# Kernel optimization log

Measured on AMD Instinct MI355X. Metric: run time of the kernel, lower is better.

Reference implementation:

```python
import jax, jax.numpy as jnp
import numpy as np

E, L, M, F, S, P = 4, 10, 512, 128, 1000, 10  # envs, labels, max_sample, features, sample_size, batch_len


def setup_inputs() -> dict:
    key = jax.random.key(0)
    k1, k2, k3 = jax.random.split(key, 3)
    data_len = jax.random.randint(k1, (E, L), M // 2, M + 1, dtype=jnp.int32)
    matrix = jax.random.normal(k2, (E, L, M, F), dtype=jnp.float32)
    # zero out padded samples beyond data_len (as shape_to_matrix does)
    pad_mask = jnp.arange(M)[None, None, :, None] < data_len[:, :, None, None]
    matrix = matrix * pad_mask
    params = jnp.eye(F, dtype=jnp.float32) + 0.01 * jax.random.normal(k3, (F, F), dtype=jnp.float32)
    is_train_env = jnp.array([True, True, False, False])
    return {"matrix": matrix, "params": params, "data_len": data_len, "is_train_env": is_train_env}


def reference(matrix, params, data_len, is_train_env):
    lenf = data_len.astype(matrix.dtype)  # [E,L], torch keeps this as float32
    # __init__ preprocessing: normalize by mean std over sample dim (detached in torch)
    std = jax.lax.stop_gradient(jnp.std(matrix, axis=2).mean())
    mat = matrix / std
    # Silverman-style bandwidth on the normalized matrix (detached in torch)
    bw = jax.lax.stop_gradient(1.06 * (M ** (-1.0 / 5.0)) * jnp.std(mat, axis=2).mean())
    offset = jnp.exp(-0.5 / bw ** 2)
    proj = jnp.einsum('elmf,fg->elmg', mat, params)  # [E,L,M,F]
    left = jax.lax.stop_gradient(proj.min())   # .item() in torch -> constant
    right = jax.lax.stop_gradient(proj.max())
    delta = (right - left) / S
    x_grid = jnp.linspace(left, right, S)
    divisor = jnp.sqrt(2.0 * jnp.pi) * bw

    def step(acc, points):  # points: [P] grid chunk
        d2 = (proj[..., None] - points) ** 2                     # [E,L,M,F,P]
        s = jnp.sum(offset ** d2, axis=2)                        # [E,L,F,P]
        # remove contribution of zero-padded samples, then normalize by true count
        corr = (M - lenf)[:, :, None] * (offset ** (points ** 2))[None, None, :]  # [E,L,P]
        r = (s - corr[:, :, None, :]) / lenf[:, :, None, None]   # [E,L,F,P]
        d = jnp.sum(jnp.abs(r[:, None] - r[None, :]), axis=-1)   # [E,E,L,F] pairwise L1 over grid chunk
        return acc + d, None

    store_dis, _ = jax.lax.scan(step, jnp.zeros((E, E, L, F), proj.dtype), x_grid.reshape(S // P, P))
    store_dis = store_dis / divisor  # [E,E,L,F]

    idx = jnp.arange(E)
    upper = idx[:, None] < idx[None, :]                                   # all env pairs i<j
    train_pair = upper & is_train_env[:, None] & is_train_env[None, :]    # train env pairs i<j
    half = store_dis * (delta / 2.0)
    neg = jnp.array(-jnp.inf, half.dtype)
    test_results = jnp.where(upper[:, :, None, None], half, neg).max(axis=(0, 1))        # [L,F]
    train_results = jnp.where(train_pair[:, :, None, None], half, neg).max(axis=(0, 1))  # [L,F]
    train_dis = train_results.max(axis=0).mean()
    test_dis = test_results.max(axis=0).mean()
    return train_results, test_results, train_dis, test_dis
```

## Files before the change

kernel.cpp:

```cpp
#include <hip/hip_runtime.h>
#include <cmath>

#define E_ 4
#define L_ 10
#define M_ 512
#define F_ 128
#define S_ 1000

typedef unsigned int u32;
typedef _Float16 f16;
typedef __attribute__((ext_vector_type(8))) _Float16 v8h;
typedef __attribute__((ext_vector_type(4))) float v4f;

__device__ __forceinline__ float fexp2(float a){
#if __has_builtin(__builtin_amdgcn_exp2f)
  return __builtin_amdgcn_exp2f(a);
#else
  return exp2f(a);
#endif
}


__global__ __launch_bounds__(256) void k_pre(const float* __restrict__ mat,
                       const float* __restrict__ par,
                       float* __restrict__ projT, float* __restrict__ wsf){
  __shared__ float sm[2048];
  int b = blockIdx.x, tid = threadIdx.x;
  if (b >= 1280){
    int el = b - 1280;
    int fq = (tid & 31) * 4, part = tid >> 5;
    const float* base = mat + ((size_t)el * M_ + part*64) * F_;
    float4 s  = make_float4(0.f,0.f,0.f,0.f);
    float4 s2 = make_float4(0.f,0.f,0.f,0.f);
    #pragma unroll 8
    for (int i = 0; i < 64; i++){
      float4 v = *(const float4*)&base[i*F_ + fq];
      s.x += v.x; s.y += v.y; s.z += v.z; s.w += v.w;
      s2.x += v.x*v.x; s2.y += v.y*v.y; s2.z += v.z*v.z; s2.w += v.w*v.w;
    }
    ((float4*)sm)[tid]       = s;
    ((float4*)sm)[256 + tid] = s2;
    __syncthreads();
    for (int g = 4; g >= 1; g >>= 1){
      if (part < g){
        float4 o  = ((float4*)sm)[tid + g*32];
        float4 o2 = ((float4*)sm)[256 + tid + g*32];
        s.x += o.x; s.y += o.y; s.z += o.z; s.w += o.w;
        s2.x += o2.x; s2.y += o2.y; s2.z += o2.z; s2.w += o2.w;
        ((float4*)sm)[tid] = s;
        ((float4*)sm)[256 + tid] = s2;
      }
      __syncthreads();
    }
    if (part == 0){
      *(float4*)&wsf[2576 + el*128 + fq] = s;
      *(float4*)&wsf[7696 + el*128 + fq] = s2;
    }
    return;
  }
  int el = b >> 5, mt = (b & 31) * 16;
  int lane = tid & 63, wave = tid >> 6;
  int q = (lane >> 4) & 3, m16 = lane & 15;
  const float* arow = mat + ((size_t)el * M_ + mt + m16) * F_;
  v4f acc0 = {0.f,0.f,0.f,0.f}, acc1 = {0.f,0.f,0.f,0.f};
  #pragma unroll
  for (int c = 0; c < 4; c++){
    float4 a0 = *(const float4*)&arow[c*32 + q*8];
    float4 a1 = *(const float4*)&arow[c*32 + q*8 + 4];
    v8h af, b0, b1;
    af[0]=(f16)a0.x; af[1]=(f16)a0.y; af[2]=(f16)a0.z; af[3]=(f16)a0.w;
    af[4]=(f16)a1.x; af[5]=(f16)a1.y; af[6]=(f16)a1.z; af[7]=(f16)a1.w;
    const float* pb = par + (c*32 + q*8)*F_ + wave*32 + m16;
    #pragma unroll
    for (int j = 0; j < 8; j++){
      b0[j] = (f16)pb[j*F_];
      b1[j] = (f16)pb[j*F_ + 16];
    }
    acc0 = __builtin_amdgcn_mfma_f32_16x16x32_f16(af, b0, acc0, 0, 0, 0);
    acc1 = __builtin_amdgcn_mfma_f32_16x16x32_f16(af, b1, acc1, 0, 0, 0);
  }
  *(float4*)(projT + ((size_t)el*F_ + wave*32      + m16)*M_ + mt + q*4)
      = make_float4(acc0[0], acc0[1], acc0[2], acc0[3]);
  *(float4*)(projT + ((size_t)el*F_ + wave*32 + 16 + m16)*M_ + mt + q*4)
      = make_float4(acc1[0], acc1[1], acc1[2], acc1[3]);
  float lmin =  3.4e38f, lmax = -3.4e38f;
  #pragma unroll
  for (int r = 0; r < 4; r++){
    lmin = fminf(lmin, fminf(acc0[r], acc1[r]));
    lmax = fmaxf(lmax, fmaxf(acc0[r], acc1[r]));
  }
  #pragma unroll
  for (int d = 32; d >= 1; d >>= 1){
    lmin = fminf(lmin, __shfl_xor(lmin, d, 64));
    lmax = fmaxf(lmax, __shfl_xor(lmax, d, 64));
  }
  if (lane == 0){ sm[wave] = lmin; sm[8+wave] = lmax; }
  __syncthreads();
  if (tid == 0){
    wsf[16   + b] = fminf(fminf(sm[0], sm[1]), fminf(sm[2], sm[3]));
    wsf[1296 + b] = fmaxf(fmaxf(sm[8], sm[9]), fmaxf(sm[10], sm[11]));
  }
}

__global__ __launch_bounds__(1024) void k_red(float* __restrict__ wsf,
                                              float divisor, float k2c){
  __shared__ float rmn[1024], rmx[1024], rs[1024];
  int tid = threadIdx.x;
  float mn = 3.4e38f, mx = -3.4e38f, s = 0.f;
  for (int i = tid; i < 1280; i += 1024){
    mn = fminf(mn, wsf[16   + i]);
    mx = fmaxf(mx, wsf[1296 + i]);
  }
  for (int i = tid; i < 5120; i += 1024){
    float a  = wsf[2576 + i];
    float a2 = wsf[7696 + i];
    float mean = a * (1.0f/512.0f);
    float var  = a2 * (1.0f/512.0f) - mean*mean;
    s += sqrtf(fmaxf(var, 0.0f));
  }
  rmn[tid] = mn; rmx[tid] = mx; rs[tid] = s;
  __syncthreads();
  for (int g = 512; g >= 1; g >>= 1){
    if (tid < g){
      rmn[tid] = fminf(rmn[tid], rmn[tid+g]);
      rmx[tid] = fmaxf(rmx[tid], rmx[tid+g]);
      rs[tid] += rs[tid+g];
    }
    __syncthreads();
  }
  float rstd   = 5120.0f / rs[0];
  float leftS  = rmn[0] * rstd;
  float rightS = rmx[0] * rstd;
  float stepFS = (rightS - leftS) * (1.0f/999.0f);
  if (tid == 0){
    float inv2 = 1.0f / (2.0f * stepFS);
    wsf[0] = rstd * inv2;
    wsf[1] = leftS * inv2;
    wsf[2] = stepFS;
    wsf[3] = leftS;
    wsf[8] = ((rightS - leftS) * (1.0f/1000.0f)) * 0.5f / divisor;
  }
  float sh = 2.0f * stepFS;
  if (tid < 152){
    float v = 0.f;
    if (tid >= 8){
      int pr = (tid >> 1) - 4;
      int u  = pr - 34;
      float d = (tid & 1) ? (float)(2*u-1) * sh : (float)(2*u) * sh;
      v = (pr < 69) ? fexp2(k2c*d*d) : 0.f;
    }
    wsf[16 + tid] = v;
  }
  if (tid >= 256 && tid < 512){
    int idx = tid - 256;
    float xc = fmaf((float)(idx - 1), 4.0f*stepFS, leftS);
    wsf[168 + idx] = fexp2(k2c * xc * xc);
  }
}

__global__ __launch_bounds__(256) void k_kde(const float* __restrict__ projT,
                      const int* __restrict__ dlen, const float* __restrict__ wsf,
                      float* __restrict__ dpair){
  __shared__ __align__(16) float smem[4752];
  int b = blockIdx.x;
  int l = b >> 7, f = b & 127;
  int tid = threadIdx.x, wave = tid >> 6, lane = tid & 63;
  int e = wave;
  const float4* gp = (const float4*)(projT + (((size_t)e * L_ + l) * F_ + f) * M_);
  float4 g0 = gp[lane], g1 = gp[lane + 64];
  float posScale = wsf[0], posOff = wsf[1];
  float lenE = (float)dlen[e*L_ + l];
  for (int idx = tid; idx < 824; idx += 256)
    ((float4*)(smem + 1024))[idx] = make_float4(0.f,0.f,0.f,0.f);
  if (tid < 38)
    ((float4*)(smem + 4320))[tid] = ((const float4*)(wsf + 16))[tid];
  if (tid >= 64 && tid < 128)
    ((float4*)(smem + 4472))[tid - 64] = ((const float4*)(wsf + 168))[tid - 64];
  __syncthreads();
  {
    float* hf = smem + 1024 + e*824;
    float pv[8] = {g0.x,g0.y,g0.z,g0.w,g1.x,g1.y,g1.z,g1.w};
    #pragma unroll
    for (int i = 0; i < 8; i++){
      float pos = fmaf(pv[i], posScale, -posOff);
      float n = floorf(pos + 0.5f);
      float d = pos - n;
      float wm = 0.5f*(0.5f-d)*(0.5f-d);
      float wp = 0.5f*(0.5f+d)*(0.5f+d);
      float w0 = 0.75f - d*d;
      int b0 = (int)n + 71;
      int b1 = b0 + 1, b2 = b0 + 2;
      int W0 = b0 + ((b0>>3)<<1);
      int W1 = b1 + ((b1>>3)<<1);
      int W2 = b2 + ((b2>>3)<<1);
      atomicAdd(&hf[W0], wm);
      atomicAdd(&hf[W1], w0);
      atomicAdd(&hf[W2], wp);
    }
  }
  __syncthreads();
  float rlen = 1.0f / lenE;
  float padc = 512.0f - lenE;
  {
    const float2* sK2 = (const float2*)(smem + 4320);
    const float* hl = smem + 1024 + e*824 + 10*lane;
    float2 c0 = sK2[72], c1 = sK2[73], c2 = sK2[74], c3 = sK2[75];
    float a0=0.f, a1=0.f, a2=0.f, a3=0.f;
    #pragma unroll
    for (int g = 0; g < 9; g++){
      float2 Hb[8];
      #pragma unroll
      for (int j = 0; j < 8; j++){
        int i = g*8 + j + 1;
        Hb[j] = *(const float2*)&hl[2*i + 2*(i>>2)];
      }
      __builtin_amdgcn_sched_group_barrier(0x100, 8, 0);
      #pragma unroll
      for (int j = 0; j < 8; j++){
        int i = g*8 + j + 1;
        a0 = fmaf(Hb[j].x, c0.x, fmaf(Hb[j].y, c0.y, a0));
        a1 = fmaf(Hb[j].x, c1.x, fmaf(Hb[j].y, c1.y, a1));
        a2 = fmaf(Hb[j].x, c2.x, fmaf(Hb[j].y, c2.y, a2));
        a3 = fmaf(Hb[j].x, c3.x, fmaf(Hb[j].y, c3.y, a3));
        c3 = c2; c2 = c1; c1 = c0; c0 = sK2[72 - i];
      }
    }
    int o0 = 4*lane;
    float4 cr = *(const float4*)&smem[4472 + o0];
    float4 stv = make_float4((a0 - padc*cr.x)*rlen, (a1 - padc*cr.y)*rlen,
                             (a2 - padc*cr.z)*rlen, (a3 - padc*cr.w)*rlen);
    *(float4*)&smem[e*256 + o0] = stv;
  }
  __syncthreads();
  float ps[6] = {0,0,0,0,0,0};
  if (tid < 250){
    float x[4][4];
    #pragma unroll
    for (int ee=0; ee<4; ee++){
      const float* st = &smem[ee*256 + tid];
      x[ee][0]=st[0]; x[ee][1]=st[1]; x[ee][2]=st[2]; x[ee][3]=st[3];
    }
    __builtin_amdgcn_sched_group_barrier(0x100, 16, 0);
    #pragma unroll
    for (int k=0; k<4; k++){
      float u = (float)k * 0.25f;
      float um1 = u - 1.0f, um2 = u - 2.0f, up1 = u + 1.0f;
      float w0 = -u * um1 * um2 * (1.0f/6.0f);
      float w1 = up1 * um1 * um2 * 0.5f;
      float w2 = -u * up1 * um2 * 0.5f;
      float w3 = u * up1 * um1 * (1.0f/6.0f);
      float rr[4];
      #pragma unroll
      for (int ee=0; ee<4; ee++)
        rr[ee] = w0*x[ee][0] + w1*x[ee][1] + w2*x[ee][2] + w3*x[ee][3];
      ps[0] += fabsf(rr[0]-rr[1]);
      ps[1] += fabsf(rr[0]-rr[2]);
      ps[2] += fabsf(rr[0]-rr[3]);
      ps[3] += fabsf(rr[1]-rr[2]);
      ps[4] += fabsf(rr[1]-rr[3]);
      ps[5] += fabsf(rr[2]-rr[3]);
    }
  }
  #pragma unroll
  for (int pr=0; pr<6; pr++){
    float v = ps[pr];
    #pragma unroll
    for (int d=32; d>=1; d>>=1) v += __shfl_xor(v, d, 64);
    if (lane == 0) smem[4728 + wave*6 + pr] = v;
  }
  __syncthreads();
  if (tid < 6)
    dpair[tid*1280 + b] = smem[4728+tid] + smem[4734+tid] + smem[4740+tid] + smem[4746+tid];
}

__global__ void k_fin(const float* __restrict__ dpair, const float* __restrict__ wsf,
                      const int* __restrict__ istrain, float* __restrict__ out){
  __shared__ float str[1280], ste[1280];
  __shared__ float s1[128], s2[128];
  int tid = threadIdx.x;
  float hscale = wsf[8];
  bool t0 = istrain[0]!=0, t1 = istrain[1]!=0, t2 = istrain[2]!=0, t3 = istrain[3]!=0;
  bool trn[6] = { t0&&t1, t0&&t2, t0&&t3, t1&&t2, t1&&t3, t2&&t3 };
  for (int idx = tid; idx < 1280; idx += 256){
    float tmax = -INFINITY, trmax = -INFINITY;
    #pragma unroll
    for (int pr=0;pr<6;pr++){
      float h = dpair[pr*1280 + idx] * hscale;
      tmax = fmaxf(tmax, h);
      if (trn[pr]) trmax = fmaxf(trmax, h);
    }
    out[idx]        = trmax;
    out[1280 + idx] = tmax;
    str[idx] = trmax; ste[idx] = tmax;
  }
  __syncthreads();
  if (tid < 128){
    float m1 = -INFINITY, m2 = -INFINITY;
    for (int l=0;l<L_;l++){
      m1 = fmaxf(m1, str[l*F_ + tid]);
      m2 = fmaxf(m2, ste[l*F_ + tid]);
    }
    s1[tid] = m1; s2[tid] = m2;
  }
  __syncthreads();
  for (int g=64; g>=1; g>>=1){
    if (tid < g){ s1[tid] += s1[tid+g]; s2[tid] += s2[tid+g]; }
    __syncthreads();
  }
  if (tid == 0){
    out[2560] = s1[0] * (1.0f/128.0f);
    out[2561] = s2[0] * (1.0f/128.0f);
  }
}

extern "C" void kernel_launch(void* const* d_in, const int* in_sizes, int n_in,
                              void* d_out, int out_size, void* d_ws, size_t ws_size,
                              hipStream_t stream){
  const float* mat = (const float*)d_in[0];
  const float* par = (const float*)d_in[1];
  const int*  dlen = (const int*)d_in[2];
  const int*  istr = (const int*)d_in[3];
  float* out   = (float*)d_out;
  float* wsf   = (float*)d_ws;
  float* dpair = wsf + 12816;
  float* projT = wsf + 20496;

  double bw_d   = 1.06 * pow(512.0, -0.2);
  float  bw     = (float)bw_d;
  float  offset = expf(-0.5f / (bw*bw));
  float  k2c    = (float)(log((double)offset) * 1.4426950408889634);
  float  divisor = sqrtf(6.283185307179586f) * bw;

  k_pre <<<1320, 256, 0, stream>>>(mat, par, projT, wsf);
  k_red <<<1,   1024, 0, stream>>>(wsf, divisor, k2c);
  k_kde <<<1280, 256, 0, stream>>>(projT, dlen, wsf, dpair);
  k_fin <<<1,    256, 0, stream>>>(dpair, wsf, istr, out);
}
```

Before: 143.2 us.

## Compute kernel tables per wave in k_kde and drop block barriers

The Gaussian kernel-weight table and the padding-correction table are no longer built once in k_red and read back from global memory. Each wave of k_kde now computes its own copy in a private LDS region. Because each wave touches only its own histogram and tables, two block-wide __syncthreads are replaced by an LDS waitcnt plus a scheduling barrier. This trims k_red's serial tail and cuts block synchronisation in k_kde, at the cost of redundant exp2 work in every wave and more LDS per block.

New measurement: 141.4 us. No clear change (-1.3%).

```diff
diff --git a/kernel.cpp b/kernel.cpp
--- a/kernel.cpp
+++ b/kernel.cpp
@@ -103,7 +103,7 @@
 }
 
 __global__ __launch_bounds__(1024) void k_red(float* __restrict__ wsf,
-                                              float divisor, float k2c){
+                                              float divisor){
   __shared__ float rmn[1024], rmx[1024], rs[1024];
   int tid = threadIdx.x;
   float mn = 3.4e38f, mx = -3.4e38f, s = 0.f;
@@ -128,55 +128,67 @@
     }
     __syncthreads();
   }
-  float rstd   = 5120.0f / rs[0];
-  float leftS  = rmn[0] * rstd;
-  float rightS = rmx[0] * rstd;
-  float stepFS = (rightS - leftS) * (1.0f/999.0f);
   if (tid == 0){
-    float inv2 = 1.0f / (2.0f * stepFS);
+    float rstd   = 5120.0f / rs[0];
+    float leftS  = rmn[0] * rstd;
+    float rightS = rmx[0] * rstd;
+    float stepFS = (rightS - leftS) * (1.0f/999.0f);
+    float inv2   = 1.0f / (2.0f * stepFS);
     wsf[0] = rstd * inv2;
     wsf[1] = leftS * inv2;
     wsf[2] = stepFS;
     wsf[3] = leftS;
     wsf[8] = ((rightS - leftS) * (1.0f/1000.0f)) * 0.5f / divisor;
   }
-  float sh = 2.0f * stepFS;
-  if (tid < 152){
-    float v = 0.f;
-    if (tid >= 8){
-      int pr = (tid >> 1) - 4;
-      int u  = pr - 34;
-      float d = (tid & 1) ? (float)(2*u-1) * sh : (float)(2*u) * sh;
-      v = (pr < 69) ? fexp2(k2c*d*d) : 0.f;
-    }
-    wsf[16 + tid] = v;
-  }
-  if (tid >= 256 && tid < 512){
-    int idx = tid - 256;
-    float xc = fmaf((float)(idx - 1), 4.0f*stepFS, leftS);
-    wsf[168 + idx] = fexp2(k2c * xc * xc);
-  }
 }
 
 __global__ __launch_bounds__(256) void k_kde(const float* __restrict__ projT,
                       const int* __restrict__ dlen, const float* __restrict__ wsf,
-                      float* __restrict__ dpair){
-  __shared__ __align__(16) float smem[4752];
+                      float* __restrict__ dpair, float k2c){
+  __shared__ __align__(16) float smem[5976];
   int b = blockIdx.x;
   int l = b >> 7, f = b & 127;
   int tid = threadIdx.x, wave = tid >> 6, lane = tid & 63;
   int e = wave;
   const float4* gp = (const float4*)(projT + (((size_t)e * L_ + l) * F_ + f) * M_);
   float4 g0 = gp[lane], g1 = gp[lane + 64];
-  float posScale = wsf[0], posOff = wsf[1];
+  float posScale = wsf[0], posOff = wsf[1], stepFS = wsf[2], leftS = wsf[3];
   float lenE = (float)dlen[e*L_ + l];
-  for (int idx = tid; idx < 824; idx += 256)
-    ((float4*)(smem + 1024))[idx] = make_float4(0.f,0.f,0.f,0.f);
-  if (tid < 38)
-    ((float4*)(smem + 4320))[tid] = ((const float4*)(wsf + 16))[tid];
-  if (tid >= 64 && tid < 128)
-    ((float4*)(smem + 4472))[tid - 64] = ((const float4*)(wsf + 168))[tid - 64];
-  __syncthreads();
+  float sh = 2.0f * stepFS;
+  {
+    float4* hz = (float4*)(smem + 1024 + e*824);
+    #pragma unroll
+    for (int i = 0; i < 4; i++){
+      int idx = lane + i*64;
+      if (idx < 206) hz[idx] = make_float4(0.f,0.f,0.f,0.f);
+    }
+  }
+  {
+    float* tw = smem + 4320 + e*152;
+    #pragma unroll
+    for (int i = 0; i < 3; i++){
+      int t = lane + i*64;
+      if (t < 152){
+        float v = 0.f;
+        if (t >= 8){
+          int pr = (t >> 1) - 4;
+          int u  = pr - 34;
+          float d = (t & 1) ? (float)(2*u-1) * sh : (float)(2*u) * sh;
+          v = (pr < 69) ? fexp2(k2c*d*d) : 0.f;
+        }
+        tw[t] = v;
+      }
+    }
+  }
+  {
+    float* cw = smem + 4928 + e*256;
+    #pragma unroll
+    for (int i = 0; i < 4; i++){
+      int t = lane + i*64;
+      float xc = fmaf((float)(t - 1), 4.0f*stepFS, leftS);
+      cw[t] = fexp2(k2c * xc * xc);
+    }
+  }
   {
     float* hf = smem + 1024 + e*824;
     float pv[8] = {g0.x,g0.y,g0.z,g0.w,g1.x,g1.y,g1.z,g1.w};
@@ -198,11 +210,12 @@
       atomicAdd(&hf[W2], wp);
     }
   }
-  __syncthreads();
+  asm volatile("s_waitcnt lgkmcnt(0)");
+  __builtin_amdgcn_sched_barrier(0);
   float rlen = 1.0f / lenE;
   float padc = 512.0f - lenE;
   {
-    const float2* sK2 = (const float2*)(smem + 4320);
+    const float2* sK2 = (const float2*)(smem + 4320 + e*152);
     const float* hl = smem + 1024 + e*824 + 10*lane;
     float2 c0 = sK2[72], c1 = sK2[73], c2 = sK2[74], c3 = sK2[75];
     float a0=0.f, a1=0.f, a2=0.f, a3=0.f;
@@ -226,7 +239,7 @@
       }
     }
     int o0 = 4*lane;
-    float4 cr = *(const float4*)&smem[4472 + o0];
+    float4 cr = *(const float4*)&smem[4928 + e*256 + o0];
     float4 stv = make_float4((a0 - padc*cr.x)*rlen, (a1 - padc*cr.y)*rlen,
                              (a2 - padc*cr.z)*rlen, (a3 - padc*cr.w)*rlen);
     *(float4*)&smem[e*256 + o0] = stv;
@@ -266,11 +279,11 @@
     float v = ps[pr];
     #pragma unroll
     for (int d=32; d>=1; d>>=1) v += __shfl_xor(v, d, 64);
-    if (lane == 0) smem[4728 + wave*6 + pr] = v;
+    if (lane == 0) smem[5952 + wave*6 + pr] = v;
   }
   __syncthreads();
   if (tid < 6)
-    dpair[tid*1280 + b] = smem[4728+tid] + smem[4734+tid] + smem[4740+tid] + smem[4746+tid];
+    dpair[tid*1280 + b] = smem[5952+tid] + smem[5958+tid] + smem[5964+tid] + smem[5970+tid];
 }
 
 __global__ void k_fin(const float* __restrict__ dpair, const float* __restrict__ wsf,
@@ -332,7 +345,7 @@
   float  divisor = sqrtf(6.283185307179586f) * bw;
 
   k_pre <<<1320, 256, 0, stream>>>(mat, par, projT, wsf);
-  k_red <<<1,   1024, 0, stream>>>(wsf, divisor, k2c);
-  k_kde <<<1280, 256, 0, stream>>>(projT, dlen, wsf, dpair);
+  k_red <<<1,   1024, 0, stream>>>(wsf, divisor);
+  k_kde <<<1280, 256, 0, stream>>>(projT, dlen, wsf, dpair, k2c);
   k_fin <<<1,    256, 0, stream>>>(dpair, wsf, istr, out);
 }
```
